# Performance work log

Measured on AMD Instinct MI355X. Metric: run time of the kernel, lower is better.

## Reference

```python
import jax, jax.numpy as jnp
import numpy as np

N, E, IN, H, C, OUT = 100000, 800000, 256, 4, 32, 64
NEG_SLOPE = 0.2


def _glorot(key, shape):
    fan = shape[0] if len(shape) > 1 else shape[-1]
    return jax.random.normal(key, shape, dtype=jnp.float32) * (1.0 / np.sqrt(fan))


def setup_inputs() -> dict:
    key = jax.random.key(0)
    ks = jax.random.split(key, 24)
    inp = {
        'x': jax.random.normal(ks[0], (N, IN), dtype=jnp.float32),
        'edge_index': jax.random.randint(ks[1], (2, E), 0, N, dtype=jnp.int64),
        # GATConv layer 0: 256 -> 4 heads x 32 (concat -> 128)
        'W0': _glorot(ks[2], (IN, H * C)), 'b0': jnp.zeros((H * C,), jnp.float32),
        'as0': _glorot(ks[3], (H, C)), 'ad0': _glorot(ks[4], (H, C)),
        # GATConv layer 1: 128 -> 4 heads x 32 (concat -> 128)
        'W1': _glorot(ks[5], (H * C, H * C)), 'b1': jnp.zeros((H * C,), jnp.float32),
        'as1': _glorot(ks[6], (H, C)), 'ad1': _glorot(ks[7], (H, C)),
        # GATConv layer 2: 128 -> 1 head x 64 (mean, concat=False)
        'W2': _glorot(ks[8], (H * C, OUT)), 'b2': jnp.zeros((OUT,), jnp.float32),
        'as2': _glorot(ks[9], (1, OUT)), 'ad2': _glorot(ks[10], (1, OUT)),
        # skip projections: layer0 Linear(256->128), layer1 Identity, layer2 Linear(128->64)
        'skip0_W': _glorot(ks[11], (IN, H * C)), 'skip0_b': jnp.zeros((H * C,), jnp.float32),
        'skip2_W': _glorot(ks[12], (H * C, OUT)), 'skip2_b': jnp.zeros((OUT,), jnp.float32),
        # JK concat linear: (128+128+64) -> 64
        'jk_W': _glorot(ks[13], (2 * H * C + OUT, OUT)), 'jk_b': jnp.zeros((OUT,), jnp.float32),
    }
    return inp


def gat_layer(x, src, dst, n, W, b, a_src, a_dst, heads, concat):
    # x: [N, F_in]; src/dst: [E'] (self-loops included); W: [F_in, heads*C]
    xh = (x @ W).reshape(n, heads, -1)                    # [N, H, C]
    al_src = jnp.einsum('nhc,hc->nh', xh, a_src)          # [N, H]
    al_dst = jnp.einsum('nhc,hc->nh', xh, a_dst)
    e = jax.nn.leaky_relu(al_src[src] + al_dst[dst], NEG_SLOPE)   # [E', H]
    emax = jax.ops.segment_max(e, dst, num_segments=n)    # self-loops => every segment nonempty
    w = jnp.exp(e - emax[dst])                            # [E', H]
    denom = jax.ops.segment_sum(w, dst, num_segments=n)   # [N, H]
    msg = xh[src] * w[:, :, None]                         # [E', H, C]
    out = jax.ops.segment_sum(msg, dst, num_segments=n) / denom[:, :, None]
    if concat:
        return out.reshape(n, -1) + b
    return out.mean(axis=1) + b


def reference(x, edge_index, W0, b0, as0, ad0, W1, b1, as1, ad1, W2, b2, as2, ad2,
              skip0_W, skip0_b, skip2_W, skip2_b, jk_W, jk_b):
    n = x.shape[0]
    loops = jnp.arange(n, dtype=edge_index.dtype)
    src = jnp.concatenate([edge_index[0], loops])
    dst = jnp.concatenate([edge_index[1], loops])
    # layer 0 (dropout is identity in eval mode)
    res0 = x @ skip0_W + skip0_b
    h = gat_layer(x, src, dst, n, W0, b0, as0, ad0, H, True) + res0
    h = jax.nn.elu(h)
    x0 = h
    # layer 1 (skip proj is Identity: 128 == 128)
    h = gat_layer(h, src, dst, n, W1, b1, as1, ad1, H, True) + h
    h = jax.nn.elu(h)
    x1 = h
    # layer 2 (1 head, concat=False -> head mean; no ELU)
    res2 = h @ skip2_W + skip2_b
    h = gat_layer(h, src, dst, n, W2, b2, as2, ad2, 1, False) + res2
    # JumpingKnowledge 'cat' + linear
    jk = jnp.concatenate([x0, x1, h], axis=-1)            # [N, 320]
    return jk @ jk_W + jk_b                               # [N, 64]
```

## Files before the change

kernel.cpp:

```cpp
#include <hip/hip_runtime.h>
#include <hip/hip_bf16.h>
#include <cstdint>

static constexpr int NN = 100000;
static constexpr int NE = 800000;
static constexpr int EP = NE + NN;
static constexpr int NB = (NN + 255) / 256;

typedef unsigned short ushort;
typedef __attribute__((ext_vector_type(8))) short short8;
typedef __attribute__((ext_vector_type(8))) ushort ushort8v;
typedef __attribute__((ext_vector_type(4))) ushort ushort4v;
typedef __attribute__((ext_vector_type(4))) float f32x4;

__device__ __forceinline__ float leaky(float x) { return x > 0.f ? x : 0.2f * x; }

__device__ __forceinline__ ushort f2bf(float f) {
    unsigned int u = __float_as_uint(f);
    u += 0x7fffu + ((u >> 16) & 1u);
    return (ushort)(u >> 16);
}
__device__ __forceinline__ float bf2f(ushort h) {
    return __uint_as_float(((unsigned int)h) << 16);
}

__global__ void pretile_kernel(const float* __restrict__ Wa, const float* __restrict__ Wb,
                               int K, int CS, int NT,
                               ushort* __restrict__ Whi, ushort* __restrict__ Wlo)
{
    int idx = blockIdx.x * 256 + threadIdx.x;
    if (idx >= K * NT) return;
    int k = idx / NT, c = idx - k * NT;
    float v = (c < CS) ? Wa[(size_t)k * CS + c] : Wb[(size_t)k * (NT - CS) + (c - CS)];
    ushort h = f2bf(v);
    ushort l = f2bf(v - bf2f(h));
    size_t o = ((size_t)(k >> 5) * NT + c) * 32 + (k & 31);
    Whi[o] = h; Wlo[o] = l;
}

template<int KTOT, int NTOT, int NCB, int K1, int K2, int CSPLIT, int BIAS_OFF,
         int AHH, int ACC, int ATTN, bool ASPLIT>
__global__ __launch_bounds__(256, 3)
void gemm_mfma(const void* __restrict__ X1, const void* __restrict__ X1b,
               const void* __restrict__ X2, const void* __restrict__ X2b,
               const void* __restrict__ X3, const void* __restrict__ X3b,
               int ldx1, int ldx2, int ldx3,
               const ushort* __restrict__ Wthi, const ushort* __restrict__ Wtlo,
               const float* __restrict__ bias,
               float* __restrict__ Y1, float* __restrict__ Y2, int ldy1, int ldy2,
               float* __restrict__ als, float* __restrict__ ald,
               const float* __restrict__ a_src, const float* __restrict__ a_dst,
               int n)
{
    constexpr int NH  = NCB / 2;
    constexpr int NF  = NH / 16;
    constexpr int NKT = KTOT / 32;

    __shared__ ushort Ahi[128][40], Alo[128][40];
    __shared__ ushort Bhi[NCB][40], Blo[NCB][40];

    const int t  = threadIdx.x;
    const int l  = t & 63, w = t >> 6;
    const int wm = w >> 1, wc = w & 1;
    const int lc = l & 15, lq = l >> 4;
    const int bm = blockIdx.x * 128;
    const int cbase = blockIdx.y * NCB;
    const int colb = wc * NH;

    f32x4 acc[4][NF];
#pragma unroll
    for (int mf = 0; mf < 4; ++mf)
#pragma unroll
        for (int nf = 0; nf < NF; ++nf)
            acc[mf][nf] = (f32x4){0.f, 0.f, 0.f, 0.f};

    const int kqf = (t & 7) * 4;
    const int rbf = t >> 3;
    const int kqs = (t & 3) * 8;
    const int rbs = t >> 2;

    float4   pa[4];
    ushort8v pah[2], pal[2];
    ushort8v pbh[NCB / 64], pbl[NCB / 64];

    auto issue = [&](int kt) {
        const int k0 = kt * 32;
        const void* xp; const void* xq; int ldx, koff;
        if (k0 < K1)      { xp = X1; xq = X1b; ldx = ldx1; koff = k0; }
        else if (k0 < K2) { xp = X2; xq = X2b; ldx = ldx2; koff = k0 - K1; }
        else              { xp = X3; xq = X3b; ldx = ldx3; koff = k0 - K2; }
        if constexpr (ASPLIT) {
            const ushort* ph = (const ushort*)xp;
            const ushort* pl = (const ushort*)xq;
#pragma unroll
            for (int p = 0; p < 2; ++p) {
                int gr = bm + rbs + p * 64;
                ushort8v zh = {0,0,0,0,0,0,0,0};
                ushort8v zl = {0,0,0,0,0,0,0,0};
                if (gr < n) {
                    size_t o = (size_t)gr * ldx + koff + kqs;
                    zh = *(const ushort8v*)&ph[o];
                    zl = *(const ushort8v*)&pl[o];
                }
                pah[p] = zh; pal[p] = zl;
            }
        } else {
            const float* pf = (const float*)xp;
#pragma unroll
            for (int p = 0; p < 4; ++p) {
                int gr = bm + rbf + p * 32;
                pa[p] = make_float4(0.f, 0.f, 0.f, 0.f);
                if (gr < n) pa[p] = *(const float4*)&pf[(size_t)gr * ldx + koff + kqf];
            }
        }
        const ushort* wb0 = &Wthi[((size_t)kt * NTOT + cbase) * 32];
        const ushort* wb1 = &Wtlo[((size_t)kt * NTOT + cbase) * 32];
#pragma unroll
        for (int ii = 0; ii < NCB / 64; ++ii) {
            int i = t + ii * 256;
            int nn = i >> 2, q = (i & 3) * 8;
            pbh[ii] = *(const ushort8v*)&wb0[nn * 32 + q];
            pbl[ii] = *(const ushort8v*)&wb1[nn * 32 + q];
        }
    };

    auto commit = [&]() {
        if constexpr (ASPLIT) {
#pragma unroll
            for (int p = 0; p < 2; ++p) {
                int rr = rbs + p * 64;
                *(ushort8v*)&Ahi[rr][kqs] = pah[p];
                *(ushort8v*)&Alo[rr][kqs] = pal[p];
            }
        } else {
#pragma unroll
            for (int p = 0; p < 4; ++p) {
                int rr = rbf + p * 32;
                ushort4v hh, ll;
                const float* vp = &pa[p].x;
#pragma unroll
                for (int e = 0; e < 4; ++e) {
                    ushort h = f2bf(vp[e]);
                    hh[e] = h;
                    ll[e] = f2bf(vp[e] - bf2f(h));
                }
                *(ushort4v*)&Ahi[rr][kqf] = hh;
                *(ushort4v*)&Alo[rr][kqf] = ll;
            }
        }
#pragma unroll
        for (int ii = 0; ii < NCB / 64; ++ii) {
            int i = t + ii * 256;
            int nn = i >> 2, q = (i & 3) * 8;
            *(ushort8v*)&Bhi[nn][q] = pbh[ii];
            *(ushort8v*)&Blo[nn][q] = pbl[ii];
        }
    };

    issue(0);
    commit();
    __syncthreads();

    for (int kt = 0; kt < NKT; ++kt) {
        const bool more = (kt + 1 < NKT);
        if (more) issue(kt + 1);

        short8 ah[4], alv[4];
#pragma unroll
        for (int mf = 0; mf < 4; ++mf) {
            ah[mf]  = *(const short8*)&Ahi[wm * 64 + mf * 16 + lc][lq * 8];
            alv[mf] = *(const short8*)&Alo[wm * 64 + mf * 16 + lc][lq * 8];
        }
#pragma unroll
        for (int nf = 0; nf < NF; ++nf) {
            short8 bh = *(const short8*)&Bhi[colb + nf * 16 + lc][lq * 8];
            short8 bl = *(const short8*)&Blo[colb + nf * 16 + lc][lq * 8];
#pragma unroll
            for (int mf = 0; mf < 4; ++mf) {
                acc[mf][nf] = __builtin_amdgcn_mfma_f32_16x16x32_bf16(ah[mf],  bh, acc[mf][nf], 0, 0, 0);
                acc[mf][nf] = __builtin_amdgcn_mfma_f32_16x16x32_bf16(ah[mf],  bl, acc[mf][nf], 0, 0, 0);
                acc[mf][nf] = __builtin_amdgcn_mfma_f32_16x16x32_bf16(alv[mf], bh, acc[mf][nf], 0, 0, 0);
            }
        }
        __syncthreads();
        if (more) {
            commit();
            __syncthreads();
        }
    }

    if constexpr (AHH > 0) {
        if (cbase == 0) {
            constexpr int FPH = ACC / 16;
            constexpr int NG  = NF / FPH;
#pragma unroll
            for (int g = 0; g < NG; ++g) {
                if (colb + g * ACC < ATTN) {
#pragma unroll
                    for (int mf = 0; mf < 4; ++mf) {
                        float ps[4] = {0.f, 0.f, 0.f, 0.f};
                        float pd[4] = {0.f, 0.f, 0.f, 0.f};
#pragma unroll
                        for (int j = 0; j < FPH; ++j) {
                            int col = colb + g * ACC + j * 16 + lc;
                            float av = a_src[col], dv = a_dst[col];
#pragma unroll
                            for (int r = 0; r < 4; ++r) {
                                ps[r] = fmaf(acc[mf][g * FPH + j][r], av, ps[r]);
                                pd[r] = fmaf(acc[mf][g * FPH + j][r], dv, pd[r]);
                            }
                        }
#pragma unroll
                        for (int off = 1; off < 16; off <<= 1)
#pragma unroll
                            for (int r = 0; r < 4; ++r) {
                                ps[r] += __shfl_xor(ps[r], off);
                                pd[r] += __shfl_xor(pd[r], off);
                            }
                        if (lc == 0) {
                            int h = (colb + g * ACC) / ACC;
#pragma unroll
                            for (int r = 0; r < 4; ++r) {
                                int row = bm + wm * 64 + mf * 16 + lq * 4 + r;
                                if (row < n) {
                                    als[(size_t)row * AHH + h] = ps[r];
                                    ald[(size_t)row * AHH + h] = pd[r];
                                }
                            }
                        }
                    }
                }
            }
        }
    }

#pragma unroll
    for (int mf = 0; mf < 4; ++mf) {
        int rowb = bm + wm * 64 + mf * 16 + lq * 4;
#pragma unroll
        for (int nf = 0; nf < NF; ++nf) {
            int col = cbase + colb + nf * 16 + lc;
            float bv = 0.f;
            if constexpr (BIAS_OFF < NTOT) {
                if (col >= BIAS_OFF) bv = bias[col - BIAS_OFF];
            }
#pragma unroll
            for (int r = 0; r < 4; ++r) {
                int row = rowb + r;
                if (row < n) {
                    float v = acc[mf][nf][r] + bv;
                    if (col < CSPLIT)
                        Y1[(size_t)row * ldy1 + col] = v;
                    else
                        Y2[(size_t)row * ldy2 + (col - CSPLIT)] = v;
                }
            }
        }
    }
}

__global__ void deg_kernel(const int* __restrict__ ei, int* __restrict__ deg)
{
    int t = blockIdx.x * blockDim.x + threadIdx.x;
    if (t < NE) atomicAdd(&deg[ei[NE + t]], 1);
}

__global__ void block_sum_kernel(const int* __restrict__ deg, int* __restrict__ bsum)
{
    int node = blockIdx.x * 256 + threadIdx.x;
    int v = (node < NN) ? deg[node] + 1 : 0;
#pragma unroll
    for (int off = 32; off > 0; off >>= 1) v += __shfl_down(v, off);
    __shared__ int sh[4];
    if ((threadIdx.x & 63) == 0) sh[threadIdx.x >> 6] = v;
    __syncthreads();
    if (threadIdx.x == 0) bsum[blockIdx.x] = sh[0] + sh[1] + sh[2] + sh[3];
}

__global__ void scan_sums_kernel(const int* __restrict__ bsum, int* __restrict__ bsumx,
                                 int* __restrict__ rowptr)
{
    if (threadIdx.x == 0) {
        int run = 0;
        for (int i = 0; i < NB; ++i) { bsumx[i] = run; run += bsum[i]; }
        rowptr[NN] = run;
    }
}

__global__ void scan_blocks_kernel(const int* __restrict__ deg, const int* __restrict__ bsumx,
                                   int* __restrict__ rowptr, int* __restrict__ cursor)
{
    __shared__ int sh[256];
    int node = blockIdx.x * 256 + threadIdx.x;
    int v = (node < NN) ? deg[node] + 1 : 0;
    sh[threadIdx.x] = v;
    __syncthreads();
#pragma unroll
    for (int off = 1; off < 256; off <<= 1) {
        int tv = (threadIdx.x >= off) ? sh[threadIdx.x - off] : 0;
        __syncthreads();
        sh[threadIdx.x] += tv;
        __syncthreads();
    }
    if (node < NN) {
        int excl = bsumx[blockIdx.x] + sh[threadIdx.x] - v;
        rowptr[node] = excl;
        cursor[node] = excl;
    }
}

__global__ void fill_kernel(const int* __restrict__ ei, int* __restrict__ cursor,
                            int* __restrict__ csr_src)
{
    int t = blockIdx.x * blockDim.x + threadIdx.x;
    if (t >= EP) return;
    int s, d;
    if (t < NE) { s = ei[t]; d = ei[NE + t]; }
    else        { s = d = t - NE; }
    int pos = atomicAdd(&cursor[d], 1);
    csr_src[pos] = s;
}

template<int HH>
__global__ __launch_bounds__(256)
void attn_weights_kernel(const int* __restrict__ rowptr, const int* __restrict__ csr_src,
                         const float* __restrict__ als, const float* __restrict__ ald,
                         float* __restrict__ wq, int n)
{
    int node = blockIdx.x * 256 + threadIdx.x;
    if (node >= n) return;
    const int e0 = rowptr[node], e1 = rowptr[node + 1];
    float aldv[HH], m[HH], d[HH];
#pragma unroll
    for (int h = 0; h < HH; ++h) { m[h] = -1e30f; d[h] = 0.f; }
    if constexpr (HH == 4) {
        float4 a = *(const float4*)&ald[(size_t)node * 4];
        aldv[0] = a.x; aldv[1] = a.y; aldv[2] = a.z; aldv[3] = a.w;
    } else {
        aldv[0] = ald[node];
    }
    for (int e = e0; e < e1; ++e) {
        int s = csr_src[e];
        float av[HH];
        if constexpr (HH == 4) {
            float4 a = *(const float4*)&als[(size_t)s * 4];
            av[0] = a.x; av[1] = a.y; av[2] = a.z; av[3] = a.w;
        } else {
            av[0] = als[s];
        }
#pragma unroll
        for (int h = 0; h < HH; ++h) {
            float sc = leaky(av[h] + aldv[h]);
            float nm = fmaxf(m[h], sc);
            d[h] = d[h] * __expf(m[h] - nm) + __expf(sc - nm);
            m[h] = nm;
        }
    }
#pragma unroll
    for (int h = 0; h < HH; ++h) d[h] = 1.f / d[h];
    for (int e = e0; e < e1; ++e) {
        int s = csr_src[e];
        float av[HH];
        if constexpr (HH == 4) {
            float4 a = *(const float4*)&als[(size_t)s * 4];
            av[0] = a.x; av[1] = a.y; av[2] = a.z; av[3] = a.w;
        } else {
            av[0] = als[s];
        }
        float wv[HH];
#pragma unroll
        for (int h = 0; h < HH; ++h)
            wv[h] = __expf(leaky(av[h] + aldv[h]) - m[h]) * d[h];
        if constexpr (HH == 4) {
            float4 o; o.x = wv[0]; o.y = wv[1]; o.z = wv[2]; o.w = wv[3];
            *(float4*)&wq[(size_t)e * 4] = o;
        } else {
            wq[e] = wv[0];
        }
    }
}

template<int HH, int CC, bool DOELU, bool RESSPLIT>
__global__ __launch_bounds__(256)
void spmm_kernel(const int* __restrict__ rowptr, const int* __restrict__ csr_src,
                 const float* __restrict__ xh, const float* __restrict__ wq,
                 const float* __restrict__ b,
                 const float* __restrict__ resf,
                 const ushort* __restrict__ resh, const ushort* __restrict__ resl,
                 ushort* __restrict__ outh, ushort* __restrict__ outl, int n)
{
    constexpr int HCL = HH * CC;
    constexpr int CPL = HCL / 64;
    const int l = threadIdx.x & 63;
    const int node = blockIdx.x * 4 + (threadIdx.x >> 6);
    if (node >= n) return;
    const int c = l * CPL;
    const int h = c / CC;
    const int e0 = rowptr[node], e1 = rowptr[node + 1];

    float a0[CPL], a1[CPL];
#pragma unroll
    for (int j = 0; j < CPL; ++j) { a0[j] = 0.f; a1[j] = 0.f; }

    int e = e0;
    for (; e + 1 < e1; e += 2) {
        int s0 = csr_src[e], s1 = csr_src[e + 1];
        float w0 = wq[(size_t)e * HH + h];
        float w1 = wq[(size_t)(e + 1) * HH + h];
        if constexpr (CPL == 2) {
            float2 x0 = *(const float2*)&xh[(size_t)s0 * HCL + c];
            float2 x1 = *(const float2*)&xh[(size_t)s1 * HCL + c];
            a0[0] = fmaf(w0, x0.x, a0[0]); a0[1] = fmaf(w0, x0.y, a0[1]);
            a1[0] = fmaf(w1, x1.x, a1[0]); a1[1] = fmaf(w1, x1.y, a1[1]);
        } else {
            a0[0] = fmaf(w0, xh[(size_t)s0 * HCL + c], a0[0]);
            a1[0] = fmaf(w1, xh[(size_t)s1 * HCL + c], a1[0]);
        }
    }
    if (e < e1) {
        int s0 = csr_src[e];
        float w0 = wq[(size_t)e * HH + h];
        if constexpr (CPL == 2) {
            float2 x0 = *(const float2*)&xh[(size_t)s0 * HCL + c];
            a0[0] = fmaf(w0, x0.x, a0[0]); a0[1] = fmaf(w0, x0.y, a0[1]);
        } else {
            a0[0] = fmaf(w0, xh[(size_t)s0 * HCL + c], a0[0]);
        }
    }

#pragma unroll
    for (int j = 0; j < CPL; ++j) {
        size_t idx = (size_t)node * HCL + c + j;
        float rv;
        if constexpr (RESSPLIT) rv = bf2f(resh[idx]) + bf2f(resl[idx]);
        else                    rv = resf[idx];
        float v = a0[j] + a1[j] + b[c + j] + rv;
        if (DOELU) v = v > 0.f ? v : (__expf(v) - 1.f);
        ushort hh = f2bf(v);
        outh[idx] = hh;
        outl[idx] = f2bf(v - bf2f(hh));
    }
}

extern "C" void kernel_launch(void* const* d_in, const int* in_sizes, int n_in,
                              void* d_out, int out_size, void* d_ws, size_t ws_size,
                              hipStream_t stream)
{
    const float* x    = (const float*)d_in[0];
    const int*   ei   = (const int*)d_in[1];
    const float* W0   = (const float*)d_in[2];
    const float* b0   = (const float*)d_in[3];
    const float* as0  = (const float*)d_in[4];
    const float* ad0  = (const float*)d_in[5];
    const float* W1   = (const float*)d_in[6];
    const float* b1   = (const float*)d_in[7];
    const float* as1  = (const float*)d_in[8];
    const float* ad1  = (const float*)d_in[9];
    const float* W2   = (const float*)d_in[10];
    const float* b2   = (const float*)d_in[11];
    const float* as2  = (const float*)d_in[12];
    const float* ad2  = (const float*)d_in[13];
    const float* sk0W = (const float*)d_in[14];
    const float* sk0b = (const float*)d_in[15];
    const float* sk2W = (const float*)d_in[16];
    const float* sk2b = (const float*)d_in[17];
    const float* jkW  = (const float*)d_in[18];
    const float* jkb  = (const float*)d_in[19];
    float* out = (float*)d_out;

    float* ws = (float*)d_ws;
    size_t off = 0;
    float* s_xh  = ws + off; off += (size_t)NN * 128;
    float* s_r0  = ws + off; off += (size_t)NN * 128;
    float* s_als = ws + off; off += (size_t)NN * 4;
    float* s_ald = ws + off; off += (size_t)NN * 4;
    float* f_wq  = ws + off; off += (size_t)EP * 4;
    ushort* u_x0h = (ushort*)(ws + off); off += (size_t)NN * 64;
    ushort* u_x0l = (ushort*)(ws + off); off += (size_t)NN * 64;
    ushort* u_x1h = (ushort*)(ws + off); off += (size_t)NN * 64;
    ushort* u_x1l = (ushort*)(ws + off); off += (size_t)NN * 64;
    ushort* u_h2h = (ushort*)(ws + off); off += (size_t)NN * 32;
    ushort* u_h2l = (ushort*)(ws + off); off += (size_t)NN * 32;
    int* i_deg    = (int*)(ws + off); off += NN;
    int* i_rowptr = (int*)(ws + off); off += NN + 1;
    int* i_cursor = (int*)(ws + off); off += NN;
    int* i_csrsrc = (int*)(ws + off); off += EP;
    int* i_bsum   = (int*)(ws + off); off += NB;
    int* i_bsumx  = (int*)(ws + off); off += NB;
    off = (off + 3) & ~(size_t)3;
    ushort* wt0h = (ushort*)(ws + off); off += 32768;
    ushort* wt0l = (ushort*)(ws + off); off += 32768;
    ushort* wt1h = (ushort*)(ws + off); off += 8192;
    ushort* wt1l = (ushort*)(ws + off); off += 8192;
    ushort* wt2h = (ushort*)(ws + off); off += 8192;
    ushort* wt2l = (ushort*)(ws + off); off += 8192;
    ushort* wtjh = (ushort*)(ws + off); off += 10240;
    ushort* wtjl = (ushort*)(ws + off); off += 10240;

    const int GM = (NN + 127) / 128;
    const int GN = (NN + 255) / 256;
    const int GS = (NN + 3) / 4;
    constexpr int BIG = 1 << 30;

    hipMemsetAsync(i_deg, 0, (size_t)NN * sizeof(int), stream);
    deg_kernel<<<(NE + 255) / 256, 256, 0, stream>>>(ei, i_deg);
    block_sum_kernel<<<NB, 256, 0, stream>>>(i_deg, i_bsum);
    scan_sums_kernel<<<1, 64, 0, stream>>>(i_bsum, i_bsumx, i_rowptr);
    scan_blocks_kernel<<<NB, 256, 0, stream>>>(i_deg, i_bsumx, i_rowptr, i_cursor);
    fill_kernel<<<(EP + 255) / 256, 256, 0, stream>>>(ei, i_cursor, i_csrsrc);

    pretile_kernel<<<256, 256, 0, stream>>>(W0, sk0W, 256, 128, 256, wt0h, wt0l);
    pretile_kernel<<<64,  256, 0, stream>>>(W1, nullptr, 128, 128, 128, wt1h, wt1l);
    pretile_kernel<<<64,  256, 0, stream>>>(W2, sk2W, 128, 64, 128, wt2h, wt2l);
    pretile_kernel<<<80,  256, 0, stream>>>(jkW, nullptr, 320, 64, 64, wtjh, wtjl);

    gemm_mfma<256, 256, 128, 256, 256, 128, 128, 4, 32, 128, false>
        <<<dim3(GM, 2), 256, 0, stream>>>(
        x, nullptr, nullptr, nullptr, nullptr, nullptr, 256, 0, 0,
        wt0h, wt0l, sk0b,
        s_xh, s_r0, 128, 128, s_als, s_ald, as0, ad0, NN);
    attn_weights_kernel<4><<<GN, 256, 0, stream>>>(
        i_rowptr, i_csrsrc, s_als, s_ald, f_wq, NN);
    spmm_kernel<4, 32, true, false><<<GS, 256, 0, stream>>>(
        i_rowptr, i_csrsrc, s_xh, f_wq, b0, s_r0, nullptr, nullptr,
        u_x0h, u_x0l, NN);

    gemm_mfma<128, 128, 128, 128, 128, 128, BIG, 4, 32, 128, true>
        <<<dim3(GM, 1), 256, 0, stream>>>(
        u_x0h, u_x0l, nullptr, nullptr, nullptr, nullptr, 128, 0, 0,
        wt1h, wt1l, nullptr,
        s_xh, nullptr, 128, 0, s_als, s_ald, as1, ad1, NN);
    attn_weights_kernel<4><<<GN, 256, 0, stream>>>(
        i_rowptr, i_csrsrc, s_als, s_ald, f_wq, NN);
    spmm_kernel<4, 32, true, true><<<GS, 256, 0, stream>>>(
        i_rowptr, i_csrsrc, s_xh, f_wq, b1, nullptr, u_x0h, u_x0l,
        u_x1h, u_x1l, NN);

    gemm_mfma<128, 128, 128, 128, 128, 64, 64, 1, 64, 64, true>
        <<<dim3(GM, 1), 256, 0, stream>>>(
        u_x1h, u_x1l, nullptr, nullptr, nullptr, nullptr, 128, 0, 0,
        wt2h, wt2l, sk2b,
        s_xh, s_r0, 64, 64, s_als, s_ald, as2, ad2, NN);
    attn_weights_kernel<1><<<GN, 256, 0, stream>>>(
        i_rowptr, i_csrsrc, s_als, s_ald, f_wq, NN);
    spmm_kernel<1, 64, false, false><<<GS, 256, 0, stream>>>(
        i_rowptr, i_csrsrc, s_xh, f_wq, b2, s_r0, nullptr, nullptr,
        u_h2h, u_h2l, NN);

    gemm_mfma<320, 64, 64, 128, 256, 64, 0, 0, 16, 0, true>
        <<<dim3(GM, 1), 256, 0, stream>>>(
        u_x0h, u_x0l, u_x1h, u_x1l, u_h2h, u_h2l, 128, 128, 64,
        wtjh, wtjl, jkb,
        out, nullptr, 64, 0, nullptr, nullptr, nullptr, nullptr, NN);
}
```

Baseline: 651.1 us.

## Load GEMM operands directly into registers, dropping LDS staging and block syncs

The MFMA GEMM no longer stages A and B tiles through shared memory. Each wave now loads its own A fragments and pretiled B fragments straight from global memory into registers, double-buffered in registers. Each wave computes a fixed 64x64 tile, and the warp grid (WR x WC) is chosen per layer instead of splitting columns across blockIdx.y. This removes LDS writes and reads and the __syncthreads barriers, but gives up sharing across waves, so global and cache traffic rises. Register pressure also grows, which is why launch bounds drop to 2 blocks per SIMD.

New measurement: 709.2 us. +8.9%, slower.

```diff
diff --git a/kernel.cpp b/kernel.cpp
--- a/kernel.cpp
+++ b/kernel.cpp
@@ -9,8 +9,6 @@
 
 typedef unsigned short ushort;
 typedef __attribute__((ext_vector_type(8))) short short8;
-typedef __attribute__((ext_vector_type(8))) ushort ushort8v;
-typedef __attribute__((ext_vector_type(4))) ushort ushort4v;
 typedef __attribute__((ext_vector_type(4))) float f32x4;
 
 __device__ __forceinline__ float leaky(float x) { return x > 0.f ? x : 0.2f * x; }
@@ -38,9 +36,9 @@
     Whi[o] = h; Wlo[o] = l;
 }
 
-template<int KTOT, int NTOT, int NCB, int K1, int K2, int CSPLIT, int BIAS_OFF,
+template<int KTOT, int NTOT, int WR, int WC, int K1, int K2, int CSPLIT, int BIAS_OFF,
          int AHH, int ACC, int ATTN, bool ASPLIT>
-__global__ __launch_bounds__(256, 3)
+__global__ __launch_bounds__(256, 2)
 void gemm_mfma(const void* __restrict__ X1, const void* __restrict__ X1b,
                const void* __restrict__ X2, const void* __restrict__ X2b,
                const void* __restrict__ X3, const void* __restrict__ X3b,
@@ -52,38 +50,45 @@
                const float* __restrict__ a_src, const float* __restrict__ a_dst,
                int n)
 {
-    constexpr int NH  = NCB / 2;
-    constexpr int NF  = NH / 16;
     constexpr int NKT = KTOT / 32;
-
-    __shared__ ushort Ahi[128][40], Alo[128][40];
-    __shared__ ushort Bhi[NCB][40], Blo[NCB][40];
 
     const int t  = threadIdx.x;
     const int l  = t & 63, w = t >> 6;
-    const int wm = w >> 1, wc = w & 1;
+    const int wm = w % WR, wc = w / WR;
     const int lc = l & 15, lq = l >> 4;
-    const int bm = blockIdx.x * 128;
-    const int cbase = blockIdx.y * NCB;
-    const int colb = wc * NH;
-
-    f32x4 acc[4][NF];
+    const int rowb = blockIdx.x * (WR * 64) + wm * 64;
+    const int colw = wc * 64;
+
+    f32x4 acc[4][4];
 #pragma unroll
     for (int mf = 0; mf < 4; ++mf)
 #pragma unroll
-        for (int nf = 0; nf < NF; ++nf)
+        for (int nf = 0; nf < 4; ++nf)
             acc[mf][nf] = (f32x4){0.f, 0.f, 0.f, 0.f};
 
-    const int kqf = (t & 7) * 4;
-    const int rbf = t >> 3;
-    const int kqs = (t & 3) * 8;
-    const int rbs = t >> 2;
-
-    float4   pa[4];
-    ushort8v pah[2], pal[2];
-    ushort8v pbh[NCB / 64], pbl[NCB / 64];
-
-    auto issue = [&](int kt) {
+    int  arow[4];
+    bool aval[4];
+#pragma unroll
+    for (int mf = 0; mf < 4; ++mf) {
+        arow[mf] = rowb + mf * 16 + lc;
+        aval[mf] = arow[mf] < n;
+    }
+
+    short8 cah[4], cal[4], cbh[4], cbl[4];
+    short8 nah[4], nal[4], nbh[4], nbl[4];
+    float4 nra[4][2];
+
+    auto loadB = [&](int kt) {
+#pragma unroll
+        for (int nf = 0; nf < 4; ++nf) {
+            int col = colw + nf * 16 + lc;
+            size_t o = ((size_t)kt * NTOT + col) * 32 + lq * 8;
+            nbh[nf] = *(const short8*)&Wthi[o];
+            nbl[nf] = *(const short8*)&Wtlo[o];
+        }
+    };
+
+    auto loadA = [&](int kt) {
         const int k0 = kt * 32;
         const void* xp; const void* xq; int ldx, koff;
         if (k0 < K1)      { xp = X1; xq = X1b; ldx = ldx1; koff = k0; }
@@ -93,139 +98,104 @@
             const ushort* ph = (const ushort*)xp;
             const ushort* pl = (const ushort*)xq;
 #pragma unroll
-            for (int p = 0; p < 2; ++p) {
-                int gr = bm + rbs + p * 64;
-                ushort8v zh = {0,0,0,0,0,0,0,0};
-                ushort8v zl = {0,0,0,0,0,0,0,0};
-                if (gr < n) {
-                    size_t o = (size_t)gr * ldx + koff + kqs;
-                    zh = *(const ushort8v*)&ph[o];
-                    zl = *(const ushort8v*)&pl[o];
+            for (int mf = 0; mf < 4; ++mf) {
+                short8 zh = {0,0,0,0,0,0,0,0}, zl = {0,0,0,0,0,0,0,0};
+                if (aval[mf]) {
+                    size_t o = (size_t)arow[mf] * ldx + koff + lq * 8;
+                    zh = *(const short8*)&ph[o];
+                    zl = *(const short8*)&pl[o];
                 }
-                pah[p] = zh; pal[p] = zl;
+                nah[mf] = zh; nal[mf] = zl;
             }
         } else {
             const float* pf = (const float*)xp;
 #pragma unroll
-            for (int p = 0; p < 4; ++p) {
-                int gr = bm + rbf + p * 32;
-                pa[p] = make_float4(0.f, 0.f, 0.f, 0.f);
-                if (gr < n) pa[p] = *(const float4*)&pf[(size_t)gr * ldx + koff + kqf];
-            }
-        }
-        const ushort* wb0 = &Wthi[((size_t)kt * NTOT + cbase) * 32];
-        const ushort* wb1 = &Wtlo[((size_t)kt * NTOT + cbase) * 32];
-#pragma unroll
-        for (int ii = 0; ii < NCB / 64; ++ii) {
-            int i = t + ii * 256;
-            int nn = i >> 2, q = (i & 3) * 8;
-            pbh[ii] = *(const ushort8v*)&wb0[nn * 32 + q];
-            pbl[ii] = *(const ushort8v*)&wb1[nn * 32 + q];
+            for (int mf = 0; mf < 4; ++mf) {
+                float4 za = make_float4(0.f,0.f,0.f,0.f), zb = za;
+                if (aval[mf]) {
+                    size_t o = (size_t)arow[mf] * ldx + koff + lq * 8;
+                    za = *(const float4*)&pf[o];
+                    zb = *(const float4*)&pf[o + 4];
+                }
+                nra[mf][0] = za; nra[mf][1] = zb;
+            }
         }
     };
 
-    auto commit = [&]() {
+    auto promote = [&]() {
         if constexpr (ASPLIT) {
 #pragma unroll
-            for (int p = 0; p < 2; ++p) {
-                int rr = rbs + p * 64;
-                *(ushort8v*)&Ahi[rr][kqs] = pah[p];
-                *(ushort8v*)&Alo[rr][kqs] = pal[p];
-            }
-        } else {
-#pragma unroll
-            for (int p = 0; p < 4; ++p) {
-                int rr = rbf + p * 32;
-                ushort4v hh, ll;
-                const float* vp = &pa[p].x;
-#pragma unroll
-                for (int e = 0; e < 4; ++e) {
-                    ushort h = f2bf(vp[e]);
-                    hh[e] = h;
-                    ll[e] = f2bf(vp[e] - bf2f(h));
+            for (int mf = 0; mf < 4; ++mf) { cah[mf] = nah[mf]; cal[mf] = nal[mf]; }
+        } else {
+#pragma unroll
+            for (int mf = 0; mf < 4; ++mf) {
+                short8 h8, l8;
+#pragma unroll
+                for (int e = 0; e < 8; ++e) {
+                    float f = (e < 4) ? (&nra[mf][0].x)[e] : (&nra[mf][1].x)[e - 4];
+                    ushort hh = f2bf(f);
+                    h8[e] = (short)hh;
+                    l8[e] = (short)f2bf(f - bf2f(hh));
                 }
-                *(ushort4v*)&Ahi[rr][kqf] = hh;
-                *(ushort4v*)&Alo[rr][kqf] = ll;
-            }
-        }
-#pragma unroll
-        for (int ii = 0; ii < NCB / 64; ++ii) {
-            int i = t + ii * 256;
-            int nn = i >> 2, q = (i & 3) * 8;
-            *(ushort8v*)&Bhi[nn][q] = pbh[ii];
-            *(ushort8v*)&Blo[nn][q] = pbl[ii];
-        }
+                cah[mf] = h8; cal[mf] = l8;
+            }
+        }
+#pragma unroll
+        for (int nf = 0; nf < 4; ++nf) { cbh[nf] = nbh[nf]; cbl[nf] = nbl[nf]; }
     };
 
-    issue(0);
-    commit();
-    __syncthreads();
-
+    loadA(0); loadB(0);
+    promote();
+
+#pragma unroll
     for (int kt = 0; kt < NKT; ++kt) {
-        const bool more = (kt + 1 < NKT);
-        if (more) issue(kt + 1);
-
-        short8 ah[4], alv[4];
-#pragma unroll
-        for (int mf = 0; mf < 4; ++mf) {
-            ah[mf]  = *(const short8*)&Ahi[wm * 64 + mf * 16 + lc][lq * 8];
-            alv[mf] = *(const short8*)&Alo[wm * 64 + mf * 16 + lc][lq * 8];
-        }
-#pragma unroll
-        for (int nf = 0; nf < NF; ++nf) {
-            short8 bh = *(const short8*)&Bhi[colb + nf * 16 + lc][lq * 8];
-            short8 bl = *(const short8*)&Blo[colb + nf * 16 + lc][lq * 8];
+        if (kt + 1 < NKT) { loadA(kt + 1); loadB(kt + 1); }
+#pragma unroll
+        for (int nf = 0; nf < 4; ++nf)
 #pragma unroll
             for (int mf = 0; mf < 4; ++mf) {
-                acc[mf][nf] = __builtin_amdgcn_mfma_f32_16x16x32_bf16(ah[mf],  bh, acc[mf][nf], 0, 0, 0);
-                acc[mf][nf] = __builtin_amdgcn_mfma_f32_16x16x32_bf16(ah[mf],  bl, acc[mf][nf], 0, 0, 0);
-                acc[mf][nf] = __builtin_amdgcn_mfma_f32_16x16x32_bf16(alv[mf], bh, acc[mf][nf], 0, 0, 0);
-            }
-        }
-        __syncthreads();
-        if (more) {
-            commit();
-            __syncthreads();
-        }
+                acc[mf][nf] = __builtin_amdgcn_mfma_f32_16x16x32_bf16(cah[mf], cbh[nf], acc[mf][nf], 0, 0, 0);
+                acc[mf][nf] = __builtin_amdgcn_mfma_f32_16x16x32_bf16(cah[mf], cbl[nf], acc[mf][nf], 0, 0, 0);
+                acc[mf][nf] = __builtin_amdgcn_mfma_f32_16x16x32_bf16(cal[mf], cbh[nf], acc[mf][nf], 0, 0, 0);
+            }
+        if (kt + 1 < NKT) promote();
     }
 
     if constexpr (AHH > 0) {
-        if (cbase == 0) {
-            constexpr int FPH = ACC / 16;
-            constexpr int NG  = NF / FPH;
-#pragma unroll
-            for (int g = 0; g < NG; ++g) {
-                if (colb + g * ACC < ATTN) {
-#pragma unroll
-                    for (int mf = 0; mf < 4; ++mf) {
-                        float ps[4] = {0.f, 0.f, 0.f, 0.f};
-                        float pd[4] = {0.f, 0.f, 0.f, 0.f};
-#pragma unroll
-                        for (int j = 0; j < FPH; ++j) {
-                            int col = colb + g * ACC + j * 16 + lc;
-                            float av = a_src[col], dv = a_dst[col];
-#pragma unroll
-                            for (int r = 0; r < 4; ++r) {
-                                ps[r] = fmaf(acc[mf][g * FPH + j][r], av, ps[r]);
-                                pd[r] = fmaf(acc[mf][g * FPH + j][r], dv, pd[r]);
-                            }
+        constexpr int FPH = ACC / 16;
+        constexpr int NG  = 64 / ACC;
+#pragma unroll
+        for (int g = 0; g < NG; ++g) {
+            if (colw + g * ACC < ATTN) {
+#pragma unroll
+                for (int mf = 0; mf < 4; ++mf) {
+                    float ps[4] = {0.f, 0.f, 0.f, 0.f};
+                    float pd[4] = {0.f, 0.f, 0.f, 0.f};
+#pragma unroll
+                    for (int j = 0; j < FPH; ++j) {
+                        int col = colw + g * ACC + j * 16 + lc;
+                        float av = a_src[col], dv = a_dst[col];
+#pragma unroll
+                        for (int r = 0; r < 4; ++r) {
+                            ps[r] = fmaf(acc[mf][g * FPH + j][r], av, ps[r]);
+                            pd[r] = fmaf(acc[mf][g * FPH + j][r], dv, pd[r]);
                         }
-#pragma unroll
-                        for (int off = 1; off < 16; off <<= 1)
-#pragma unroll
-                            for (int r = 0; r < 4; ++r) {
-                                ps[r] += __shfl_xor(ps[r], off);
-                                pd[r] += __shfl_xor(pd[r], off);
-                            }
-                        if (lc == 0) {
-                            int h = (colb + g * ACC) / ACC;
-#pragma unroll
-                            for (int r = 0; r < 4; ++r) {
-                                int row = bm + wm * 64 + mf * 16 + lq * 4 + r;
-                                if (row < n) {
-                                    als[(size_t)row * AHH + h] = ps[r];
-                                    ald[(size_t)row * AHH + h] = pd[r];
-                                }
+                    }
+#pragma unroll
+                    for (int off = 1; off < 16; off <<= 1)
+#pragma unroll
+                        for (int r = 0; r < 4; ++r) {
+                            ps[r] += __shfl_xor(ps[r], off);
+                            pd[r] += __shfl_xor(pd[r], off);
+                        }
+                    if (lc == 0) {
+                        int h = (colw + g * ACC) / ACC;
+#pragma unroll
+                        for (int r = 0; r < 4; ++r) {
+                            int row = rowb + mf * 16 + lq * 4 + r;
+                            if (row < n) {
+                                als[(size_t)row * AHH + h] = ps[r];
+                                ald[(size_t)row * AHH + h] = pd[r];
                             }
                         }
                     }
@@ -236,23 +206,23 @@
 
 #pragma unroll
     for (int mf = 0; mf < 4; ++mf) {
-        int rowb = bm + wm * 64 + mf * 16 + lq * 4;
-#pragma unroll
-        for (int nf = 0; nf < NF; ++nf) {
-            int col = cbase + colb + nf * 16 + lc;
+        int rb4 = rowb + mf * 16 + lq * 4;
+#pragma unroll
+        for (int nf = 0; nf < 4; ++nf) {
+            int col = colw + nf * 16 + lc;
             float bv = 0.f;
             if constexpr (BIAS_OFF < NTOT) {
                 if (col >= BIAS_OFF) bv = bias[col - BIAS_OFF];
             }
 #pragma unroll
             for (int r = 0; r < 4; ++r) {
-                int row = rowb + r;
+                int row = rb4 + r;
                 if (row < n) {
                     float v = acc[mf][nf][r] + bv;
                     if (col < CSPLIT)
-                        Y1[(size_t)row * ldy1 + col] = v;
+                        *(&Y1[(size_t)row * ldy1 + col]) = v;
                     else
-                        Y2[(size_t)row * ldy2 + (col - CSPLIT)] = v;
+                        *(&Y2[(size_t)row * ldy2 + (col - CSPLIT)]) = v;
                 }
             }
         }
@@ -497,7 +467,10 @@
     ushort* wtjh = (ushort*)(ws + off); off += 10240;
     ushort* wtjl = (ushort*)(ws + off); off += 10240;
 
-    const int GM = (NN + 127) / 128;
+    const int GM64  = (NN + 63) / 256 * 4 + (((NN % 256) + 63) / 64);
+    const int G64   = (NN + 63) / 64;
+    const int G128  = (NN + 127) / 128;
+    const int G256  = (NN + 255) / 256;
     const int GN = (NN + 255) / 256;
     const int GS = (NN + 3) / 4;
     constexpr int BIG = 1 << 30;
@@ -514,8 +487,8 @@
     pretile_kernel<<<64,  256, 0, stream>>>(W2, sk2W, 128, 64, 128, wt2h, wt2l);
     pretile_kernel<<<80,  256, 0, stream>>>(jkW, nullptr, 320, 64, 64, wtjh, wtjl);
 
-    gemm_mfma<256, 256, 128, 256, 256, 128, 128, 4, 32, 128, false>
-        <<<dim3(GM, 2), 256, 0, stream>>>(
+    gemm_mfma<256, 256, 1, 4, 256, 256, 128, 128, 4, 32, 128, false>
+        <<<G64, 256, 0, stream>>>(
         x, nullptr, nullptr, nullptr, nullptr, nullptr, 256, 0, 0,
         wt0h, wt0l, sk0b,
         s_xh, s_r0, 128, 128, s_als, s_ald, as0, ad0, NN);
@@ -525,8 +498,8 @@
         i_rowptr, i_csrsrc, s_xh, f_wq, b0, s_r0, nullptr, nullptr,
         u_x0h, u_x0l, NN);
 
-    gemm_mfma<128, 128, 128, 128, 128, 128, BIG, 4, 32, 128, true>
-        <<<dim3(GM, 1), 256, 0, stream>>>(
+    gemm_mfma<128, 128, 2, 2, 128, 128, 128, BIG, 4, 32, 128, true>
+        <<<G128, 256, 0, stream>>>(
         u_x0h, u_x0l, nullptr, nullptr, nullptr, nullptr, 128, 0, 0,
         wt1h, wt1l, nullptr,
         s_xh, nullptr, 128, 0, s_als, s_ald, as1, ad1, NN);
@@ -536,8 +509,8 @@
         i_rowptr, i_csrsrc, s_xh, f_wq, b1, nullptr, u_x0h, u_x0l,
         u_x1h, u_x1l, NN);
 
-    gemm_mfma<128, 128, 128, 128, 128, 64, 64, 1, 64, 64, true>
-        <<<dim3(GM, 1), 256, 0, stream>>>(
+    gemm_mfma<128, 128, 2, 2, 128, 128, 64, 64, 1, 64, 64, true>
+        <<<G128, 256, 0, stream>>>(
         u_x1h, u_x1l, nullptr, nullptr, nullptr, nullptr, 128, 0, 0,
         wt2h, wt2l, sk2b,
         s_xh, s_r0, 64, 64, s_als, s_ald, as2, ad2, NN);
@@ -547,8 +520,8 @@
         i_rowptr, i_csrsrc, s_xh, f_wq, b2, s_r0, nullptr, nullptr,
         u_h2h, u_h2l, NN);
 
-    gemm_mfma<320, 64, 64, 128, 256, 64, 0, 0, 16, 0, true>
-        <<<dim3(GM, 1), 256, 0, stream>>>(
+    gemm_mfma<320, 64, 4, 1, 128, 256, 64, 0, 0, 16, 0, true>
+        <<<G256, 256, 0, stream>>>(
         u_x0h, u_x0l, u_x1h, u_x1l, u_h2h, u_h2l, 128, 128, 64,
         wtjh, wtjl, jkb,
         out, nullptr, 64, 0, nullptr, nullptr, nullptr, nullptr, NN);
```
